# Performance work log

Hardware: AMD Instinct MI355X
Metric: run time of the kernel (lower is better)

## Reference

```python
import jax, jax.numpy as jnp
import numpy as np

N = 128   # n_features == out_dim (required by the Christoffel permutes)
H = 256   # MLP hidden width of forward_func
B = 16    # batch size (state_batch is [2B, N])
EPS_G = 1e-4
EPS_DG = 1e-6
EPS_V = 1e-6


def setup_inputs() -> dict:
    key = jax.random.key(0)
    ks = jax.random.split(key, 6)
    return {
        "t": jax.random.uniform(ks[0], (), dtype=jnp.float32),
        "state_batch": jax.random.normal(ks[1], (2 * B, N), dtype=jnp.float32) * 0.1,
        "x0_batch": jax.random.normal(ks[2], (B, N), dtype=jnp.float32),
        "x1_batch": jax.random.normal(ks[3], (B, N), dtype=jnp.float32),
        "W1": jax.random.normal(ks[4], (N, H), dtype=jnp.float32) / np.float32(np.sqrt(N)),
        "b1": jnp.zeros((H,), dtype=jnp.float32),
        "W2": jax.random.normal(ks[5], (H, N), dtype=jnp.float32) / np.float32(np.sqrt(H)),
        "b2": jnp.zeros((N,), dtype=jnp.float32),
    }


def reference(t, state_batch, x0_batch, x1_batch, W1, b1, W2, b2):
    def f(x):  # forward_func, per-sample: [N] -> [N]
        return jnp.tanh(x @ W1 + b1) @ W2 + b2

    def metric(x):  # G(x) = J J^T + 1e-4 I, per-sample: [N] -> [N, N]
        J = jax.jacrev(f)(x)                      # [N, N], matches per-output grad loop
        return J @ J.T + EPS_G * jnp.eye(N, dtype=x.dtype)

    deviation, dev_velocity = jnp.split(state_batch, 2, axis=0)  # each [B, N]
    window = 4.0 * t * (1.0 - t)
    # x along the perturbed straight path
    x = x0_batch + t * (x1_batch - x0_batch) + window * deviation  # [B, N]

    # dG[b, i, j, k] = dG_ij/dx_k -- replaces the out_dim^2 autograd.grad loop
    dG = jax.vmap(jax.jacfwd(metric))(x)  # [B, N, N, N]
    nrm = jnp.sqrt(jnp.sum(dG * dG, axis=(1, 2, 3), keepdims=True))
    dG = dG / (nrm + EPS_DG)

    # Christoffel-like symbols
    Gamma = 0.5 * (dG + jnp.transpose(dG, (0, 2, 1, 3)) - jnp.transpose(dG, (0, 3, 1, 2)))
    a = -jnp.einsum('bijk,bj,bk->bi', Gamma, dev_velocity, dev_velocity)
    a = a / (jnp.linalg.norm(dev_velocity, axis=1, keepdims=True) + EPS_V)

    restoration = -0.1 * deviation
    return jnp.concatenate([dev_velocity, a + restoration], axis=0)  # [2B, N]
```

## Files before the change

### kernel.cpp

```cpp
#include <hip/hip_runtime.h>
#include <math.h>


static constexpr int OFF_W2T  = 0;
static constexpr int OFF_S    = 32768;
static constexpr int OFF_Q    = 98304;
static constexpr int OFF_D    = 163840;
static constexpr int OFF_C    = 167936;
static constexpr int OFF_UV   = 172032;
static constexpr int OFF_AV   = 176128;
static constexpr int OFF_VN   = 180224;
static constexpr int OFF_SUM  = 180240;
static constexpr int OFF_CNT  = 180256;
static constexpr int OFF_PT   = 180288;
static constexpr int OFF_PN   = OFF_PT + 16 * 32768;

__global__ __launch_bounds__(256) void k_stage1c(const float* __restrict__ tptr,
                                                 const float* __restrict__ state,
                                                 const float* __restrict__ x0,
                                                 const float* __restrict__ x1,
                                                 const float* __restrict__ W1,
                                                 const float* __restrict__ b1,
                                                 const float* __restrict__ W2,
                                                 float* __restrict__ ws,
                                                 float* __restrict__ out) {
    __shared__ __align__(16) float lds[8192];
    int blk = blockIdx.x;
    int tid = threadIdx.x;

    if (blk < 64) {
        float* Ai = lds;
        float* Aj = lds + 1088;
        int m0 = (blk >> 3) * 32, n0 = (blk & 7) * 32;
        int lx = tid & 31, lr = tid >> 5;
        int tx = tid & 15, ty = tid >> 4;
        float a00 = 0, a01 = 0, a10 = 0, a11 = 0;
        for (int kc = 0; kc < 128; kc += 32) {
            #pragma unroll
            for (int i = 0; i < 4; ++i) {
                int k = lr + 8 * i;
                Ai[k * 34 + lx] = W1[(kc + k) * 256 + m0 + lx];
                Aj[k * 34 + lx] = W1[(kc + k) * 256 + n0 + lx];
            }
            __syncthreads();
            #pragma unroll
            for (int k = 0; k < 32; ++k) {
                float2 a = *(const float2*)&Ai[k * 34 + 2 * ty];
                float2 b = *(const float2*)&Aj[k * 34 + 2 * tx];
                a00 += a.x * b.x; a01 += a.x * b.y;
                a10 += a.y * b.x; a11 += a.y * b.y;
            }
            __syncthreads();
        }
        float* S = ws + OFF_S;
        int m = m0 + 2 * ty, n = n0 + 2 * tx;
        S[m * 256 + n]           = a00;
        S[m * 256 + n + 1]       = a01;
        S[(m + 1) * 256 + n]     = a10;
        S[(m + 1) * 256 + n + 1] = a11;
    } else if (blk < 96) {
        int bqq = blk - 64;
        for (int hh = 0; hh < 2; ++hh) {
            int bq = bqq + 32 * hh;
            float* Xi = lds;
            float* Xj = lds + 1088;
            int m0 = (bq >> 3) * 32, n0 = (bq & 7) * 32;
            int lx = tid & 31, lr = tid >> 5;
            int tx = tid & 15, ty = tid >> 4;
            float a00 = 0, a01 = 0, a10 = 0, a11 = 0;
            for (int kc = 0; kc < 128; kc += 32) {
                #pragma unroll
                for (int i = 0; i < 4; ++i) {
                    Xi[lx * 34 + lr + 8 * i] = W2[(m0 + lr + 8 * i) * 128 + kc + lx];
                    Xj[lx * 34 + lr + 8 * i] = W2[(n0 + lr + 8 * i) * 128 + kc + lx];
                }
                __syncthreads();
                #pragma unroll
                for (int k = 0; k < 32; ++k) {
                    float2 a = *(const float2*)&Xi[k * 34 + 2 * ty];
                    float2 b = *(const float2*)&Xj[k * 34 + 2 * tx];
                    a00 += a.x * b.x; a01 += a.x * b.y;
                    a10 += a.y * b.x; a11 += a.y * b.y;
                }
                __syncthreads();
            }
            float* Q = ws + OFF_Q;
            int m = m0 + 2 * ty, n = n0 + 2 * tx;
            Q[m * 256 + n]           = a00;
            Q[m * 256 + n + 1]       = a01;
            Q[(m + 1) * 256 + n]     = a10;
            Q[(m + 1) * 256 + n + 1] = a11;
            __syncthreads();
        }
    } else if (blk < 112) {
        int bt = blk - 96;
        for (int hh = 0; hh < 2; ++hh) {
            int b2 = bt + 16 * hh;
            float* tile = lds;
            int c0 = (b2 & 3) * 32, r0 = (b2 >> 2) * 32;
            int tx = tid & 31, ty = tid >> 5;
            #pragma unroll
            for (int i = 0; i < 32; i += 8)
                tile[(ty + i) * 33 + tx] = W2[(r0 + ty + i) * 128 + c0 + tx];
            __syncthreads();
            float* W2T = ws + OFF_W2T;
            #pragma unroll
            for (int i = 0; i < 32; i += 8)
                W2T[(c0 + ty + i) * 256 + r0 + tx] = tile[tx * 33 + ty + i];
            __syncthreads();
        }
    } else if (blk < 128) {
        int b = blk - 112;
        float* xs  = lds;
        float* vs  = lds + 128;
        float* red = lds + 256;
        float t = tptr[0];
        float w = 4.f * t * (1.f - t);
        if (tid == 0) {
            ws[OFF_SUM + b] = 0.f;
            ((int*)ws)[OFF_CNT + b] = 0;
        }
        if (tid < 128) {
            float dev = state[b * 128 + tid];
            float v   = state[(16 + b) * 128 + tid];
            float xv  = x0[b * 128 + tid] + t * (x1[b * 128 + tid] - x0[b * 128 + tid]) + w * dev;
            xs[tid] = xv;
            vs[tid] = v;
            out[b * 128 + tid] = v;
            red[tid] = v * v;
        }
        __syncthreads();
        for (int s = 64; s > 0; s >>= 1) {
            if (tid < s) red[tid] += red[tid + s];
            __syncthreads();
        }
        if (tid == 0) ws[OFF_VN + b] = sqrtf(red[0]);

        int m = tid;
        float h = b1[m], uvm = 0.f;
        #pragma unroll 8
        for (int k = 0; k < 128; ++k) {
            float wv = W1[k * 256 + m];
            h   += xs[k] * wv;
            uvm += vs[k] * wv;
        }
        float z  = tanhf(h);
        float dd = 1.f - z * z;
        float cc = -2.f * z * dd;
        const float4* w2r = (const float4*)&W2[m * 128];
        const float4* vs4 = (const float4*)vs;
        float avm = 0.f;
        #pragma unroll 8
        for (int j4 = 0; j4 < 32; ++j4) {
            float4 ww = w2r[j4];
            float4 vv = vs4[j4];
            avm += ww.x * vv.x + ww.y * vv.y + ww.z * vv.z + ww.w * vv.w;
        }
        ws[OFF_D  + b * 256 + m] = dd;
        ws[OFF_C  + b * 256 + m] = cc;
        ws[OFF_UV + b * 256 + m] = uvm;
        ws[OFF_AV + b * 256 + m] = avm;
    } else {
        int q = blk - 128;
        int b = q >> 4, jt = q & 15, j0 = jt * 8;
        float* xs  = lds;
        float* dsv = lds + 128;
        float* W1s = lds + 384;
        float* YdT = lds + 4992;
        float* Fl  = lds + 5280;
        float t = tptr[0];
        float w = 4.f * t * (1.f - t);
        if (tid < 128) {
            float dev = state[b * 128 + tid];
            xs[tid] = x0[b * 128 + tid] + t * (x1[b * 128 + tid] - x0[b * 128 + tid]) + w * dev;
        }
        __syncthreads();
        {
            int m = tid;
            float h = b1[m];
            #pragma unroll 8
            for (int k = 0; k < 128; ++k) h += xs[k] * W1[k * 256 + m];
            float z = tanhf(h);
            dsv[m] = 1.f - z * z;
        }
        __syncthreads();

        float facc[4] = {};
        int pj = tid & 7, pk = tid >> 3;
        for (int nc = 0; nc < 256; nc += 32) {
            {
                int r = tid >> 1, h16 = (tid & 1) * 16;
                #pragma unroll
                for (int c = 0; c < 4; ++c)
                    *(float4*)&W1s[r * 36 + h16 + 4 * c] =
                        *(const float4*)&W1[r * 256 + nc + h16 + 4 * c];
            }
            if (tid < 64) {
                int n2 = tid >> 1, c4 = (tid & 1) * 4;
                float4 wv = *(const float4*)&W2[(nc + n2) * 128 + j0 + c4];
                float dn = dsv[nc + n2];
                YdT[(c4 + 0) * 36 + n2] = wv.x * dn;
                YdT[(c4 + 1) * 36 + n2] = wv.y * dn;
                YdT[(c4 + 2) * 36 + n2] = wv.z * dn;
                YdT[(c4 + 3) * 36 + n2] = wv.w * dn;
            }
            __syncthreads();
            #pragma unroll
            for (int nn = 0; nn < 32; nn += 4) {
                float4 yv = *(const float4*)&YdT[pj * 36 + nn];
                #pragma unroll
                for (int kk = 0; kk < 4; ++kk) {
                    float4 wv = *(const float4*)&W1s[(pk + 32 * kk) * 36 + nn];
                    facc[kk] += wv.x * yv.x; facc[kk] += wv.y * yv.y;
                    facc[kk] += wv.z * yv.z; facc[kk] += wv.w * yv.w;
                }
            }
            __syncthreads();
        }
        #pragma unroll
        for (int kk = 0; kk < 4; ++kk)
            Fl[(pk + 32 * kk) * 12 + pj] = facc[kk];
        __syncthreads();

        float acc2[8] = {};
        int m = tid;
        #pragma unroll 4
        for (int k = 0; k < 128; ++k) {
            float wv = W1[k * 256 + m];
            float4 f0 = *(const float4*)&Fl[k * 12];
            float4 f1 = *(const float4*)&Fl[k * 12 + 4];
            acc2[0] += wv * f0.x; acc2[1] += wv * f0.y;
            acc2[2] += wv * f0.z; acc2[3] += wv * f0.w;
            acc2[4] += wv * f1.x; acc2[5] += wv * f1.y;
            acc2[6] += wv * f1.z; acc2[7] += wv * f1.w;
        }
        float* ptb = ws + OFF_PT + b * 32768;
        float* pnb = ws + OFF_PN + b * 32768;
        #pragma unroll
        for (int jj = 0; jj < 8; ++jj)
            ptb[(j0 + jj) * 256 + m] = acc2[jj];
        *(float4*)&pnb[m * 128 + j0]     = make_float4(acc2[0], acc2[1], acc2[2], acc2[3]);
        *(float4*)&pnb[m * 128 + j0 + 4] = make_float4(acc2[4], acc2[5], acc2[6], acc2[7]);
    }
}

__global__ __launch_bounds__(256, 4) void k_fnorm7(const float* __restrict__ state,
                                                   const float* __restrict__ W2,
                                                   float* __restrict__ ws,
                                                   float* __restrict__ out) {
    __shared__ __align__(16) float lds[9408];
    int blk = blockIdx.x;
    int tid = threadIdx.x;
    int* cnt = (int*)ws + OFF_CNT;

    if (blk < 16) {
        int b = blk;
        const float* ptb = ws + OFF_PT + b * 32768;
        const float* pnb = ws + OFF_PN + b * 32768;
        float* vs   = lds;
        float* g1   = lds + 128;
        float* g2   = lds + 384;
        float* red  = lds + 640;
        float* snrm = lds + 900;
        if (tid < 128) vs[tid] = state[(16 + b) * 128 + tid];
        __syncthreads();

        int m = tid;
        float pv = 0.f;
        #pragma unroll 8
        for (int j = 0; j < 128; ++j)
            pv += ptb[j * 256 + m] * vs[j];
        float cc  = ws[OFF_C  + b * 256 + m];
        float uvm = ws[OFF_UV + b * 256 + m];
        float avm = ws[OFF_AV + b * 256 + m];
        g1[m] = cc * pv  * uvm;
        g2[m] = cc * avm * uvm;
        __syncthreads();

        int i = tid & 127, half = tid >> 7;
        int mmlo = half * 128;
        float raw = 0.f;
        #pragma unroll 8
        for (int mm = mmlo; mm < mmlo + 128; ++mm)
            raw += W2[mm * 128 + i] * g1[mm] + pnb[mm * 128 + i] * g2[mm];
        red[tid] = raw;
        __syncthreads();

        if (tid == 0) {
            while (atomicAdd(&cnt[b], 0) < 36) __builtin_amdgcn_s_sleep(2);
            __threadfence();
            float tot = atomicAdd(&ws[OFF_SUM + b], 0.0f);
            snrm[0] = sqrtf(fmaxf(2.f * tot, 0.f));
        }
        __syncthreads();
        if (tid < 128) {
            float rawt = red[tid] + red[tid + 128];
            float vn = ws[OFF_VN + b];
            float a  = -0.5f * rawt / ((snrm[0] + 1e-6f) * (vn + 1e-6f));
            out[(16 + b) * 128 + tid] = a - 0.1f * state[b * 128 + tid];
        }
        return;
    }

    int q   = blk - 16;
    int idx = q >> 4;
    int b   = q & 15;
    int tj = 0;
    while ((tj + 1) * (tj + 2) / 2 <= idx) ++tj;
    int ti = idx - tj * (tj + 1) / 2;
    int mi0 = ti * 32, mj0 = tj * 32;
    float* PiT = lds;
    float* PjT = lds + 2048;
    float* WiT = lds + 4096;
    float* WjT = lds + 6144;
    const float* ptb  = ws + OFF_PT + b * 32768;
    const float* W2T  = ws + OFF_W2T;
    const float* Smat = ws + OFF_S;
    const float* Qmat = ws + OFF_Q;
    int jr = tid >> 3, jc4 = (tid & 7) * 4;
    int w = tid >> 6, s = tid & 63;
    int ty = s >> 3, tx = s & 7;
    float r[4][4] = {}, f[4][4] = {}, g[4][4] = {};
    #pragma unroll
    for (int rr = 0; rr < 2; ++rr) {
        #pragma unroll
        for (int it = 0; it < 2; ++it) {
            int l = jr + 32 * it;
            int j = 32 * (l >> 4) + 16 * rr + (l & 15);
            *(float4*)&PiT[l * 32 + jc4] = *(const float4*)&ptb[j * 256 + mi0 + jc4];
            *(float4*)&PjT[l * 32 + jc4] = *(const float4*)&ptb[j * 256 + mj0 + jc4];
            *(float4*)&WiT[l * 32 + jc4] = *(const float4*)&W2T[j * 256 + mi0 + jc4];
            *(float4*)&WjT[l * 32 + jc4] = *(const float4*)&W2T[j * 256 + mj0 + jc4];
        }
        __syncthreads();
        #pragma unroll 4
        for (int jj = 0; jj < 16; ++jj) {
            int l = 16 * w + jj;
            float4 pi4 = *(const float4*)&PiT[l * 32 + 4 * ty];
            float4 pj4 = *(const float4*)&PjT[l * 32 + 4 * tx];
            float4 wi4 = *(const float4*)&WiT[l * 32 + 4 * ty];
            float4 wj4 = *(const float4*)&WjT[l * 32 + 4 * tx];
            float pi[4] = {pi4.x, pi4.y, pi4.z, pi4.w};
            float pj[4] = {pj4.x, pj4.y, pj4.z, pj4.w};
            float wi[4] = {wi4.x, wi4.y, wi4.z, wi4.w};
            float wj[4] = {wj4.x, wj4.y, wj4.z, wj4.w};
            #pragma unroll
            for (int ii = 0; ii < 4; ++ii)
                #pragma unroll
                for (int kk = 0; kk < 4; ++kk) {
                    r[ii][kk] += pi[ii] * pj[kk];
                    f[ii][kk] += pi[ii] * wj[kk];
                    g[ii][kk] += pj[kk] * wi[ii];
                }
        }
        __syncthreads();
    }
    if (w != 0) {
        float* scr = lds;
        int base = ((w - 1) * 64 + s) * 49;
        #pragma unroll
        for (int ii = 0; ii < 4; ++ii)
            #pragma unroll
            for (int kk = 0; kk < 4; ++kk) {
                scr[base + ii * 4 + kk]      = r[ii][kk];
                scr[base + 16 + ii * 4 + kk] = f[ii][kk];
                scr[base + 32 + ii * 4 + kk] = g[ii][kk];
            }
    }
    __syncthreads();
    if (tid < 64) {
        float tr[16], tf[16], tg[16];
        #pragma unroll
        for (int ii = 0; ii < 4; ++ii)
            #pragma unroll
            for (int kk = 0; kk < 4; ++kk) {
                tr[ii * 4 + kk] = r[ii][kk];
                tf[ii * 4 + kk] = f[ii][kk];
                tg[ii * 4 + kk] = g[ii][kk];
            }
        for (int ww = 0; ww < 3; ++ww) {
            const float* sc = lds + (ww * 64 + tid) * 49;
            #pragma unroll
            for (int k = 0; k < 16; ++k) {
                tr[k] += sc[k];
                tf[k] += sc[16 + k];
                tg[k] += sc[32 + k];
            }
        }
        const float* cb = ws + OFF_C + b * 256;
        int mi = mi0 + 4 * (tid >> 3), mj = mj0 + 4 * (tid & 7);
        float4 ce4 = *(const float4*)&cb[mj];
        float ce[4] = {ce4.x, ce4.y, ce4.z, ce4.w};
        float sum = 0.f;
        #pragma unroll
        for (int ii = 0; ii < 4; ++ii) {
            float ci = cb[mi + ii];
            float4 S4 = *(const float4*)&Smat[(mi + ii) * 256 + mj];
            float4 Q4 = *(const float4*)&Qmat[(mi + ii) * 256 + mj];
            float Sv[4] = {S4.x, S4.y, S4.z, S4.w};
            float Qv[4] = {Q4.x, Q4.y, Q4.z, Q4.w};
            #pragma unroll
            for (int kk = 0; kk < 4; ++kk)
                sum += ci * ce[kk] * Sv[kk] * (Qv[kk] * tr[ii * 4 + kk] + tf[ii * 4 + kk] * tg[ii * 4 + kk]);
        }
        if (ti < tj) sum *= 2.f;
        #pragma unroll
        for (int off = 32; off > 0; off >>= 1)
            sum += __shfl_down(sum, off);
        if (tid == 0) {
            atomicAdd(&ws[OFF_SUM + b], sum);
            __threadfence();
            atomicAdd(&cnt[b], 1);
        }
    }
}

extern "C" void kernel_launch(void* const* d_in, const int* in_sizes, int n_in,
                              void* d_out, int out_size, void* d_ws, size_t ws_size,
                              hipStream_t stream) {
    (void)in_sizes; (void)n_in; (void)out_size; (void)ws_size;
    const float* t     = (const float*)d_in[0];
    const float* state = (const float*)d_in[1];
    const float* x0    = (const float*)d_in[2];
    const float* x1    = (const float*)d_in[3];
    const float* W1    = (const float*)d_in[4];
    const float* b1    = (const float*)d_in[5];
    const float* W2    = (const float*)d_in[6];
    float* out = (float*)d_out;
    float* ws  = (float*)d_ws;

    k_stage1c<<<384, 256, 0, stream>>>(t, state, x0, x1, W1, b1, W2, ws, out);
    k_fnorm7<<<592, 256, 0, stream>>>(state, W2, ws, out);
}
```

Before: 112.4 us.

## Split stage1 work across more blocks and prefetch next tile in fnorm

Stage-one blocks that looped twice over the Q and W2-transpose tiles are unrolled so that each block does one tile. The per-sample P computation is split into 32 column groups of 4 instead of 16 of 8, raising the grid from 384 to 688 blocks. In the fnorm kernel, global loads for the second half of the tile go into registers before the compute on the first half, so load latency overlaps with math. The extra blocks recompute the hidden layer redundantly, and the prefetch raises register pressure.

```diff
diff --git a/kernel.cpp b/kernel.cpp
--- a/kernel.cpp
+++ b/kernel.cpp
@@ -15,7 +15,7 @@
 static constexpr int OFF_PT   = 180288;
 static constexpr int OFF_PN   = OFF_PT + 16 * 32768;
 
-__global__ __launch_bounds__(256) void k_stage1c(const float* __restrict__ tptr,
+__global__ __launch_bounds__(256) void k_stage1d(const float* __restrict__ tptr,
                                                  const float* __restrict__ state,
                                                  const float* __restrict__ x0,
                                                  const float* __restrict__ x1,
@@ -58,59 +58,51 @@
         S[m * 256 + n + 1]       = a01;
         S[(m + 1) * 256 + n]     = a10;
         S[(m + 1) * 256 + n + 1] = a11;
-    } else if (blk < 96) {
-        int bqq = blk - 64;
-        for (int hh = 0; hh < 2; ++hh) {
-            int bq = bqq + 32 * hh;
-            float* Xi = lds;
-            float* Xj = lds + 1088;
-            int m0 = (bq >> 3) * 32, n0 = (bq & 7) * 32;
-            int lx = tid & 31, lr = tid >> 5;
-            int tx = tid & 15, ty = tid >> 4;
-            float a00 = 0, a01 = 0, a10 = 0, a11 = 0;
-            for (int kc = 0; kc < 128; kc += 32) {
-                #pragma unroll
-                for (int i = 0; i < 4; ++i) {
-                    Xi[lx * 34 + lr + 8 * i] = W2[(m0 + lr + 8 * i) * 128 + kc + lx];
-                    Xj[lx * 34 + lr + 8 * i] = W2[(n0 + lr + 8 * i) * 128 + kc + lx];
-                }
-                __syncthreads();
-                #pragma unroll
-                for (int k = 0; k < 32; ++k) {
-                    float2 a = *(const float2*)&Xi[k * 34 + 2 * ty];
-                    float2 b = *(const float2*)&Xj[k * 34 + 2 * tx];
-                    a00 += a.x * b.x; a01 += a.x * b.y;
-                    a10 += a.y * b.x; a11 += a.y * b.y;
-                }
-                __syncthreads();
-            }
-            float* Q = ws + OFF_Q;
-            int m = m0 + 2 * ty, n = n0 + 2 * tx;
-            Q[m * 256 + n]           = a00;
-            Q[m * 256 + n + 1]       = a01;
-            Q[(m + 1) * 256 + n]     = a10;
-            Q[(m + 1) * 256 + n + 1] = a11;
-            __syncthreads();
-        }
-    } else if (blk < 112) {
-        int bt = blk - 96;
-        for (int hh = 0; hh < 2; ++hh) {
-            int b2 = bt + 16 * hh;
-            float* tile = lds;
-            int c0 = (b2 & 3) * 32, r0 = (b2 >> 2) * 32;
-            int tx = tid & 31, ty = tid >> 5;
-            #pragma unroll
-            for (int i = 0; i < 32; i += 8)
-                tile[(ty + i) * 33 + tx] = W2[(r0 + ty + i) * 128 + c0 + tx];
-            __syncthreads();
-            float* W2T = ws + OFF_W2T;
-            #pragma unroll
-            for (int i = 0; i < 32; i += 8)
-                W2T[(c0 + ty + i) * 256 + r0 + tx] = tile[tx * 33 + ty + i];
-            __syncthreads();
-        }
     } else if (blk < 128) {
-        int b = blk - 112;
+        int bq = blk - 64;
+        float* Xi = lds;
+        float* Xj = lds + 1088;
+        int m0 = (bq >> 3) * 32, n0 = (bq & 7) * 32;
+        int lx = tid & 31, lr = tid >> 5;
+        int tx = tid & 15, ty = tid >> 4;
+        float a00 = 0, a01 = 0, a10 = 0, a11 = 0;
+        for (int kc = 0; kc < 128; kc += 32) {
+            #pragma unroll
+            for (int i = 0; i < 4; ++i) {
+                Xi[lx * 34 + lr + 8 * i] = W2[(m0 + lr + 8 * i) * 128 + kc + lx];
+                Xj[lx * 34 + lr + 8 * i] = W2[(n0 + lr + 8 * i) * 128 + kc + lx];
+            }
+            __syncthreads();
+            #pragma unroll
+            for (int k = 0; k < 32; ++k) {
+                float2 a = *(const float2*)&Xi[k * 34 + 2 * ty];
+                float2 b = *(const float2*)&Xj[k * 34 + 2 * tx];
+                a00 += a.x * b.x; a01 += a.x * b.y;
+                a10 += a.y * b.x; a11 += a.y * b.y;
+            }
+            __syncthreads();
+        }
+        float* Q = ws + OFF_Q;
+        int m = m0 + 2 * ty, n = n0 + 2 * tx;
+        Q[m * 256 + n]           = a00;
+        Q[m * 256 + n + 1]       = a01;
+        Q[(m + 1) * 256 + n]     = a10;
+        Q[(m + 1) * 256 + n + 1] = a11;
+    } else if (blk < 160) {
+        int b2 = blk - 128;
+        float* tile = lds;
+        int c0 = (b2 & 3) * 32, r0 = (b2 >> 2) * 32;
+        int tx = tid & 31, ty = tid >> 5;
+        #pragma unroll
+        for (int i = 0; i < 32; i += 8)
+            tile[(ty + i) * 33 + tx] = W2[(r0 + ty + i) * 128 + c0 + tx];
+        __syncthreads();
+        float* W2T = ws + OFF_W2T;
+        #pragma unroll
+        for (int i = 0; i < 32; i += 8)
+            W2T[(c0 + ty + i) * 256 + r0 + tx] = tile[tx * 33 + ty + i];
+    } else if (blk < 176) {
+        int b = blk - 160;
         float* xs  = lds;
         float* vs  = lds + 128;
         float* red = lds + 256;
@@ -161,13 +153,13 @@
         ws[OFF_UV + b * 256 + m] = uvm;
         ws[OFF_AV + b * 256 + m] = avm;
     } else {
-        int q = blk - 128;
-        int b = q >> 4, jt = q & 15, j0 = jt * 8;
+        int q = blk - 176;
+        int b = q >> 5, jt = q & 31, j0 = jt * 4;
         float* xs  = lds;
         float* dsv = lds + 128;
         float* W1s = lds + 384;
         float* YdT = lds + 4992;
-        float* Fl  = lds + 5280;
+        float* Fl  = lds + 5136;
         float t = tptr[0];
         float w = 4.f * t * (1.f - t);
         if (tid < 128) {
@@ -185,8 +177,8 @@
         }
         __syncthreads();
 
-        float facc[4] = {};
-        int pj = tid & 7, pk = tid >> 3;
+        float facc[2] = {};
+        int pj = tid & 3, pk = tid >> 2;
         for (int nc = 0; nc < 256; nc += 32) {
             {
                 int r = tid >> 1, h16 = (tid & 1) * 16;
@@ -195,22 +187,22 @@
                     *(float4*)&W1s[r * 36 + h16 + 4 * c] =
                         *(const float4*)&W1[r * 256 + nc + h16 + 4 * c];
             }
-            if (tid < 64) {
-                int n2 = tid >> 1, c4 = (tid & 1) * 4;
-                float4 wv = *(const float4*)&W2[(nc + n2) * 128 + j0 + c4];
+            if (tid < 32) {
+                int n2 = tid;
+                float4 wv = *(const float4*)&W2[(nc + n2) * 128 + j0];
                 float dn = dsv[nc + n2];
-                YdT[(c4 + 0) * 36 + n2] = wv.x * dn;
-                YdT[(c4 + 1) * 36 + n2] = wv.y * dn;
-                YdT[(c4 + 2) * 36 + n2] = wv.z * dn;
-                YdT[(c4 + 3) * 36 + n2] = wv.w * dn;
+                YdT[0 * 36 + n2] = wv.x * dn;
+                YdT[1 * 36 + n2] = wv.y * dn;
+                YdT[2 * 36 + n2] = wv.z * dn;
+                YdT[3 * 36 + n2] = wv.w * dn;
             }
             __syncthreads();
             #pragma unroll
             for (int nn = 0; nn < 32; nn += 4) {
                 float4 yv = *(const float4*)&YdT[pj * 36 + nn];
                 #pragma unroll
-                for (int kk = 0; kk < 4; ++kk) {
-                    float4 wv = *(const float4*)&W1s[(pk + 32 * kk) * 36 + nn];
+                for (int kk = 0; kk < 2; ++kk) {
+                    float4 wv = *(const float4*)&W1s[(pk + 64 * kk) * 36 + nn];
                     facc[kk] += wv.x * yv.x; facc[kk] += wv.y * yv.y;
                     facc[kk] += wv.z * yv.z; facc[kk] += wv.w * yv.w;
                 }
@@ -218,33 +210,29 @@
             __syncthreads();
         }
         #pragma unroll
-        for (int kk = 0; kk < 4; ++kk)
-            Fl[(pk + 32 * kk) * 12 + pj] = facc[kk];
-        __syncthreads();
-
-        float acc2[8] = {};
+        for (int kk = 0; kk < 2; ++kk)
+            Fl[(pk + 64 * kk) * 4 + pj] = facc[kk];
+        __syncthreads();
+
+        float acc2[4] = {};
         int m = tid;
         #pragma unroll 4
         for (int k = 0; k < 128; ++k) {
             float wv = W1[k * 256 + m];
-            float4 f0 = *(const float4*)&Fl[k * 12];
-            float4 f1 = *(const float4*)&Fl[k * 12 + 4];
+            float4 f0 = *(const float4*)&Fl[k * 4];
             acc2[0] += wv * f0.x; acc2[1] += wv * f0.y;
             acc2[2] += wv * f0.z; acc2[3] += wv * f0.w;
-            acc2[4] += wv * f1.x; acc2[5] += wv * f1.y;
-            acc2[6] += wv * f1.z; acc2[7] += wv * f1.w;
         }
         float* ptb = ws + OFF_PT + b * 32768;
         float* pnb = ws + OFF_PN + b * 32768;
         #pragma unroll
-        for (int jj = 0; jj < 8; ++jj)
+        for (int jj = 0; jj < 4; ++jj)
             ptb[(j0 + jj) * 256 + m] = acc2[jj];
-        *(float4*)&pnb[m * 128 + j0]     = make_float4(acc2[0], acc2[1], acc2[2], acc2[3]);
-        *(float4*)&pnb[m * 128 + j0 + 4] = make_float4(acc2[4], acc2[5], acc2[6], acc2[7]);
+        *(float4*)&pnb[m * 128 + j0] = make_float4(acc2[0], acc2[1], acc2[2], acc2[3]);
     }
 }
 
-__global__ __launch_bounds__(256, 4) void k_fnorm7(const float* __restrict__ state,
+__global__ __launch_bounds__(256, 4) void k_fnorm8(const float* __restrict__ state,
                                                    const float* __restrict__ W2,
                                                    float* __restrict__ ws,
                                                    float* __restrict__ out) {
@@ -321,18 +309,38 @@
     int w = tid >> 6, s = tid & 63;
     int ty = s >> 3, tx = s & 7;
     float r[4][4] = {}, f[4][4] = {}, g[4][4] = {};
+    float4 rPi[2], rPj[2], rWi[2], rWj[2];
+    #pragma unroll
+    for (int it = 0; it < 2; ++it) {
+        int l = jr + 32 * it;
+        int j = 32 * (l >> 4) + (l & 15);
+        rPi[it] = *(const float4*)&ptb[j * 256 + mi0 + jc4];
+        rPj[it] = *(const float4*)&ptb[j * 256 + mj0 + jc4];
+        rWi[it] = *(const float4*)&W2T[j * 256 + mi0 + jc4];
+        rWj[it] = *(const float4*)&W2T[j * 256 + mj0 + jc4];
+    }
     #pragma unroll
     for (int rr = 0; rr < 2; ++rr) {
         #pragma unroll
         for (int it = 0; it < 2; ++it) {
             int l = jr + 32 * it;
-            int j = 32 * (l >> 4) + 16 * rr + (l & 15);
-            *(float4*)&PiT[l * 32 + jc4] = *(const float4*)&ptb[j * 256 + mi0 + jc4];
-            *(float4*)&PjT[l * 32 + jc4] = *(const float4*)&ptb[j * 256 + mj0 + jc4];
-            *(float4*)&WiT[l * 32 + jc4] = *(const float4*)&W2T[j * 256 + mi0 + jc4];
-            *(float4*)&WjT[l * 32 + jc4] = *(const float4*)&W2T[j * 256 + mj0 + jc4];
-        }
-        __syncthreads();
+            *(float4*)&PiT[l * 32 + jc4] = rPi[it];
+            *(float4*)&PjT[l * 32 + jc4] = rPj[it];
+            *(float4*)&WiT[l * 32 + jc4] = rWi[it];
+            *(float4*)&WjT[l * 32 + jc4] = rWj[it];
+        }
+        __syncthreads();
+        if (rr == 0) {
+            #pragma unroll
+            for (int it = 0; it < 2; ++it) {
+                int l = jr + 32 * it;
+                int j = 32 * (l >> 4) + 16 + (l & 15);
+                rPi[it] = *(const float4*)&ptb[j * 256 + mi0 + jc4];
+                rPj[it] = *(const float4*)&ptb[j * 256 + mj0 + jc4];
+                rWi[it] = *(const float4*)&W2T[j * 256 + mi0 + jc4];
+                rWj[it] = *(const float4*)&W2T[j * 256 + mj0 + jc4];
+            }
+        }
         #pragma unroll 4
         for (int jj = 0; jj < 16; ++jj) {
             int l = 16 * w + jj;
@@ -429,6 +437,6 @@
     float* out = (float*)d_out;
     float* ws  = (float*)d_ws;
 
-    k_stage1c<<<384, 256, 0, stream>>>(t, state, x0, x1, W1, b1, W2, ws, out);
-    k_fnorm7<<<592, 256, 0, stream>>>(state, W2, ws, out);
+    k_stage1d<<<688, 256, 0, stream>>>(t, state, x0, x1, W1, b1, W2, ws, out);
+    k_fnorm8<<<592, 256, 0, stream>>>(state, W2, ws, out);
 }
```

Result: slower. 182.6 us (+62.4%).
